# Kernel tuning notes

Measured on AMD Instinct MI355X. Metric: run time of the kernel, lower is better.

The kernel has to match this reference:

```python
import jax, jax.numpy as jnp
import numpy as np

E = 16        # num experts
D = 1024      # d_model
F = 512       # expert intermediate dim
B, S = 2, 2048


def setup_inputs() -> dict:
    key = jax.random.key(0)
    ks = jax.random.split(key, 8)
    sc = lambda fan_in: 1.0 / np.sqrt(fan_in)
    return {
        "x": jax.random.normal(ks[0], (B, S, D), dtype=jnp.float32),
        "router_w": jax.random.normal(ks[1], (E, D), dtype=jnp.float32) * sc(D),
        "gate_w": jax.random.normal(ks[2], (E, D, F), dtype=jnp.float32) * sc(D),
        "up_w": jax.random.normal(ks[3], (E, D, F), dtype=jnp.float32) * sc(D),
        "down_w": jax.random.normal(ks[4], (E, F, D), dtype=jnp.float32) * sc(F),
        "sg_w": jax.random.normal(ks[5], (D, F), dtype=jnp.float32) * sc(D),
        "su_w": jax.random.normal(ks[6], (D, F), dtype=jnp.float32) * sc(D),
        "sd_w": jax.random.normal(ks[7], (F, D), dtype=jnp.float32) * sc(F),
        "top_k": 8,
    }


def reference(x, router_w, gate_w, up_w, down_w, sg_w, su_w, sd_w, top_k):
    shape = x.shape
    xf = x.reshape(-1, shape[-1])                      # [T, D]
    # --- router: softmax then top-k, renormalize ---
    logits = xf.astype(jnp.float32) @ router_w.T       # [T, E]
    probs = jax.nn.softmax(logits, axis=-1)
    w, idx = jax.lax.top_k(probs, top_k)               # [T, k]
    w = w / jnp.sum(w, axis=-1, keepdims=True)
    # combine weight per (token, expert): sum over the k slots
    cw = jnp.sum(jax.nn.one_hot(idx, E, dtype=w.dtype) * w[..., None], axis=1)  # [T, E]
    # --- experts (dense batched SwiGLU, weighted combine) ---
    g = jnp.einsum("td,edf->etf", xf, gate_w)          # [E, T, F]
    u = jnp.einsum("td,edf->etf", xf, up_w)
    h = jax.nn.silu(g) * u
    out = jnp.einsum("etf,efd,te->td", h, down_w, cw)  # [T, D]
    # --- shared expert ---
    out = out + (jax.nn.silu(xf @ sg_w) * (xf @ su_w)) @ sd_w
    return out.reshape(shape)
```

## Files before the change

### kernel.cpp

```cpp
#include <hip/hip_runtime.h>
#include <hip/hip_bf16.h>

#define T_TOK 4096
#define DDIM  1024
#define FDIM  512
#define NEXP  16
#define NE17  17
#define MAXTILES 304

using bf16x8 = __attribute__((ext_vector_type(8))) __bf16;
using f32x4  = __attribute__((ext_vector_type(4))) float;

__device__ __forceinline__ void gload_lds16(const void* g, void* l) {
  __builtin_amdgcn_global_load_lds(
      (const __attribute__((address_space(1))) void*)g,
      (__attribute__((address_space(3))) void*)l, 16, 0, 0);
}

__device__ __forceinline__ bf16x8 frag_ld(const __hip_bfloat16* smem, int row, int chunk) {
  const char* p = (const char*)smem + row * 128 + ((chunk ^ (row & 7)) << 4);
  return *(const bf16x8*)p;
}

__global__ void convert_router(const float* __restrict__ x, const float* __restrict__ rw,
                               __hip_bfloat16* __restrict__ xb, float* __restrict__ cw) {
  const int t = blockIdx.x;
  const int lane = threadIdx.x;
  const float4* xrow = (const float4*)(x + (size_t)t * DDIM);
  float4 v[4];
#pragma unroll
  for (int c = 0; c < 4; c++) v[c] = xrow[lane + 64 * c];
  __hip_bfloat16* orow = xb + (size_t)t * DDIM;
#pragma unroll
  for (int c = 0; c < 4; c++) {
    __hip_bfloat16 h[4] = {__float2bfloat16(v[c].x), __float2bfloat16(v[c].y),
                           __float2bfloat16(v[c].z), __float2bfloat16(v[c].w)};
    *(uint2*)(orow + (lane + 64 * c) * 4) = *(const uint2*)h;
  }
  const float4* rw4 = (const float4*)rw;
  float myLg = 0.f;
#pragma unroll
  for (int e = 0; e < NEXP; e++) {
    float p = 0.f;
#pragma unroll
    for (int c = 0; c < 4; c++) {
      const float4 r = rw4[e * 256 + lane + 64 * c];
      p += v[c].x * r.x + v[c].y * r.y + v[c].z * r.z + v[c].w * r.w;
    }
#pragma unroll
    for (int off = 32; off > 0; off >>= 1) p += __shfl_xor(p, off);
    if (lane == e) myLg = p;
  }
  float m = myLg;
#pragma unroll
  for (int off = 8; off > 0; off >>= 1) m = fmaxf(m, __shfl_xor(m, off));
  const float pe = __expf(myLg - m);
  int rank = 0;
#pragma unroll
  for (int j = 0; j < NEXP; j++) {
    const float pj = __shfl(pe, j);
    rank += ((pj > pe) || (pj == pe && j < lane)) ? 1 : 0;
  }
  const bool sel = (lane < NEXP) && (rank < 8);
  float ss = sel ? pe : 0.f;
#pragma unroll
  for (int off = 8; off > 0; off >>= 1) ss += __shfl_xor(ss, off);
  if (lane < NEXP) cw[(size_t)t * NEXP + lane] = sel ? pe / ss : 0.f;
}

__global__ void moe_count(const float* __restrict__ cw, int* __restrict__ cnt) {
  const int e = blockIdx.x;
  const int lane = threadIdx.x;
  int c = 0;
  for (int t = lane; t < T_TOK; t += 64) c += (cw[(size_t)t * 16 + e] > 0.f) ? 1 : 0;
#pragma unroll
  for (int off = 32; off > 0; off >>= 1) c += __shfl_xor(c, off);
  if (lane == 0) cnt[e] = c;
}

__global__ void moe_scan(const int* __restrict__ cnt, int* __restrict__ padBase,
                         int* __restrict__ tileE, int* __restrict__ tileBase) {
  if (threadIdx.x != 0) return;
  int base = 0, tile = 0;
  for (int e = 0; e < 16; e++) {
    padBase[e] = base;
    const int nt = (cnt[e] + 127) >> 7;
    for (int i = 0; i < nt; i++) { tileE[tile] = e; tileBase[tile] = base + (i << 7); tile++; }
    base += nt << 7;
  }
  padBase[16] = base;
  for (int i = 0; i < 32; i++) { tileE[tile] = 16; tileBase[tile] = base + (i << 7); tile++; }
  for (; tile < MAXTILES; tile++) tileE[tile] = -1;
}

__global__ void moe_place(const float* __restrict__ cw, const int* __restrict__ cnt,
                          const int* __restrict__ padBase,
                          int* __restrict__ perm, float* __restrict__ rowW) {
  const int e = blockIdx.x;
  const int lane = threadIdx.x;
  const int base = padBase[e];
  if (e == 16) {
    for (int t = lane; t < T_TOK; t += 64) { perm[base + t] = t; rowW[base + t] = 1.0f; }
    return;
  }
  int running = 0;
  for (int t0 = 0; t0 < T_TOK; t0 += 64) {
    const int t = t0 + lane;
    const float w = cw[(size_t)t * 16 + e];
    const unsigned long long m = __ballot(w > 0.f);
    if (w > 0.f) {
      const int r = base + running + __popcll(m & ((1ull << lane) - 1ull));
      perm[r] = t; rowW[r] = w;
    }
    running += __popcll(m);
  }
  const int padded = ((cnt[e] + 127) >> 7) << 7;
  for (int i = running + lane; i < padded; i += 64) { perm[base + i] = -1; rowW[base + i] = 0.f; }
}

__global__ __launch_bounds__(256, 4) void transpose_convert2(
    const float* __restrict__ srcMainA, const float* __restrict__ srcSharedA,
    const float* __restrict__ srcMainB, const float* __restrict__ srcSharedB,
    __hip_bfloat16* __restrict__ dstA, __hip_bfloat16* __restrict__ dstB, int R, int C) {
  const int e = blockIdx.z;
  const float* srcA = (e < NEXP) ? srcMainA + (size_t)e * R * C : srcSharedA;
  const float* srcB = (e < NEXP) ? srcMainB + (size_t)e * R * C : srcSharedB;
  __hip_bfloat16* outA = dstA + (size_t)e * R * C;
  __hip_bfloat16* outB = dstB + (size_t)e * R * C;
  __shared__ float tA[64][65];
  __shared__ float tB[64][65];
  const int c0 = blockIdx.x * 64, r0 = blockIdx.y * 64;
  const int tx = threadIdx.x, ty = threadIdx.y;
#pragma unroll
  for (int i = 0; i < 64; i += 4) {
    tA[ty + i][tx] = srcA[(size_t)(r0 + ty + i) * C + c0 + tx];
    tB[ty + i][tx] = srcB[(size_t)(r0 + ty + i) * C + c0 + tx];
  }
  __syncthreads();
#pragma unroll
  for (int i = 0; i < 64; i += 4) {
    outA[(size_t)(c0 + ty + i) * R + r0 + tx] = __float2bfloat16(tA[tx][ty + i]);
    outB[(size_t)(c0 + ty + i) * R + r0 + tx] = __float2bfloat16(tB[tx][ty + i]);
  }
}

__global__ __launch_bounds__(256, 4) void transpose_convert(
    const float* __restrict__ srcMain, const float* __restrict__ srcShared,
    __hip_bfloat16* __restrict__ dst, int R, int C) {
  const int e = blockIdx.z;
  const float* src = (e < NEXP) ? srcMain + (size_t)e * R * C : srcShared;
  __hip_bfloat16* out = dst + (size_t)e * R * C;
  __shared__ float tile[64][65];
  const int c0 = blockIdx.x * 64, r0 = blockIdx.y * 64;
  const int tx = threadIdx.x, ty = threadIdx.y;
#pragma unroll
  for (int i = 0; i < 64; i += 4)
    tile[ty + i][tx] = src[(size_t)(r0 + ty + i) * C + c0 + tx];
  __syncthreads();
#pragma unroll
  for (int i = 0; i < 64; i += 4)
    out[(size_t)(c0 + ty + i) * R + r0 + tx] = __float2bfloat16(tile[tx][ty + i]);
}

__global__ __launch_bounds__(256, 3) void moe_stageA_grouped(
    const __hip_bfloat16* __restrict__ xb,
    const __hip_bfloat16* __restrict__ wg,
    const __hip_bfloat16* __restrict__ wu,
    const int* __restrict__ perm, const float* __restrict__ rowW,
    const int* __restrict__ tileE, const int* __restrict__ tileBase,
    __hip_bfloat16* __restrict__ H)
{
  __shared__ __hip_bfloat16 sA[128 * 64];
  __shared__ __hip_bfloat16 sG[64 * 64];
  __shared__ __hip_bfloat16 sU[64 * 64];
  __shared__ int   sTok[128];
  __shared__ float sW[128];

  const int tile = (blockIdx.x & 7) * (MAXTILES / 8) + (blockIdx.x >> 3);
  const int e = tileE[tile];
  if (e < 0) return;
  const int rbase = tileBase[tile];
  const int f0 = blockIdx.y * 64;
  const int tid = threadIdx.x;
  const int wid = tid >> 6, lane = tid & 63;
  const int wr = (wid >> 1) * 64, wc = (wid & 1) * 32;
  const int rl = lane >> 3, cl = lane & 7;

  if (tid < 128) { const int r = rbase + tid; sTok[tid] = perm[r]; sW[tid] = rowW[r]; }
  __syncthreads();

  const __hip_bfloat16* wgE = wg + (size_t)e * FDIM * DDIM;
  const __hip_bfloat16* wuE = wu + (size_t)e * FDIM * DDIM;

  const char* pA[4]; const char* pG[2]; const char* pU[2]; int ldsA[4], ldsB[2];
#pragma unroll
  for (int i = 0; i < 4; i++) {
    const int row = 32 * wid + 8 * i + rl;
    const int sw = (cl ^ (row & 7)) << 3;
    int tk = sTok[row]; if (tk < 0) tk = 0;
    pA[i] = (const char*)(xb + (size_t)tk * DDIM + sw);
    ldsA[i] = (32 * wid + 8 * i) * 64;
  }
#pragma unroll
  for (int i = 0; i < 2; i++) {
    const int row = 16 * wid + 8 * i + rl;
    const int sw = (cl ^ (row & 7)) << 3;
    pG[i] = (const char*)(wgE + (size_t)(f0 + row) * DDIM + sw);
    pU[i] = (const char*)(wuE + (size_t)(f0 + row) * DDIM + sw);
    ldsB[i] = (16 * wid + 8 * i) * 64;
  }

  const f32x4 vzero = {0.f, 0.f, 0.f, 0.f};
  f32x4 accG[4][2], accU[4][2];
#pragma unroll
  for (int m = 0; m < 4; m++)
#pragma unroll
    for (int n = 0; n < 2; n++) { accG[m][n] = vzero; accU[m][n] = vzero; }

  for (int k0 = 0; k0 < DDIM; k0 += 64) {
    __syncthreads();
#pragma unroll
    for (int i = 0; i < 4; i++) gload_lds16(pA[i] + (size_t)k0 * 2, &sA[ldsA[i]]);
#pragma unroll
    for (int i = 0; i < 2; i++) {
      gload_lds16(pG[i] + (size_t)k0 * 2, &sG[ldsB[i]]);
      gload_lds16(pU[i] + (size_t)k0 * 2, &sU[ldsB[i]]);
    }
    __syncthreads();
#pragma unroll
    for (int kk = 0; kk < 2; kk++) {
      const int kch = kk * 4 + (lane >> 4);
      bf16x8 af[4], bg[2], bu[2];
#pragma unroll
      for (int m = 0; m < 4; m++) af[m] = frag_ld(sA, wr + m * 16 + (lane & 15), kch);
#pragma unroll
      for (int n = 0; n < 2; n++) {
        bg[n] = frag_ld(sG, wc + n * 16 + (lane & 15), kch);
        bu[n] = frag_ld(sU, wc + n * 16 + (lane & 15), kch);
      }
#pragma unroll
      for (int m = 0; m < 4; m++)
#pragma unroll
        for (int n = 0; n < 2; n++) {
          accG[m][n] = __builtin_amdgcn_mfma_f32_16x16x32_bf16(af[m], bg[n], accG[m][n], 0, 0, 0);
          accU[m][n] = __builtin_amdgcn_mfma_f32_16x16x32_bf16(af[m], bu[n], accU[m][n], 0, 0, 0);
        }
    }
  }
  const int lr = (lane >> 4) * 4, lc = lane & 15;
#pragma unroll
  for (int m = 0; m < 4; m++)
#pragma unroll
    for (int n = 0; n < 2; n++)
#pragma unroll
      for (int j = 0; j < 4; j++) {
        const int r = wr + m * 16 + lr + j;
        const int c = wc + n * 16 + lc;
        const int tok = sTok[r];
        if (tok >= 0) {
          const float g = accG[m][n][j], u = accU[m][n][j];
          const float h = (g / (1.0f + __expf(-g))) * u * sW[r];
          H[((size_t)e * T_TOK + tok) * FDIM + f0 + c] = __float2bfloat16(h);
        }
      }
}

__global__ __launch_bounds__(256, 4) void moe_stageB_split(
    const __hip_bfloat16* __restrict__ H,
    const __hip_bfloat16* __restrict__ wd,
    float* __restrict__ out,
    float* __restrict__ p0, float* __restrict__ p1)
{
  __shared__ __hip_bfloat16 sA[128 * 64];
  __shared__ __hip_bfloat16 sB[128 * 64];

  const int id = blockIdx.x;
  const int xcd = id & 7, slot = id >> 3;
  const int t0 = (xcd * 4 + (slot & 3)) * 128;
  const int d0 = (slot >> 2) * 128;
  const int tid = threadIdx.x, wid = tid >> 6, lane = tid & 63;
  const int wr = (wid >> 1) * 64, wc = (wid & 1) * 64;
  const int rl = lane >> 3, cl = lane & 7;

  size_t offA[4], offB[4]; int ldsO[4];
#pragma unroll
  for (int i = 0; i < 4; i++) {
    const int row = 32 * wid + 8 * i + rl;
    const int sw = (cl ^ (row & 7)) << 3;
    offA[i] = (size_t)(t0 + row) * FDIM + sw;
    offB[i] = (size_t)(d0 + row) * FDIM + sw;
    ldsO[i] = (32 * wid + 8 * i) * 64;
  }

  const f32x4 vzero = {0.f, 0.f, 0.f, 0.f};
  f32x4 acc[4][4];
#pragma unroll
  for (int m = 0; m < 4; m++)
#pragma unroll
    for (int n = 0; n < 4; n++) acc[m][n] = vzero;

  const int NKS = NE17 * FDIM / 64;
  const int split = blockIdx.y;
  const int ks0 = (split * NKS) / 3, ks1 = ((split + 1) * NKS) / 3;

  for (int ks = ks0; ks < ks1; ks++) {
    const int k0 = ks * 64;
    const int ee = k0 >> 9, ff = k0 & 511;
    const size_t sOffA = (size_t)ee * T_TOK * FDIM + ff;
    const size_t sOffB = (size_t)ee * DDIM * FDIM + ff;
    __syncthreads();
#pragma unroll
    for (int i = 0; i < 4; i++) {
      gload_lds16(H  + sOffA + offA[i], &sA[ldsO[i]]);
      gload_lds16(wd + sOffB + offB[i], &sB[ldsO[i]]);
    }
    __syncthreads();
#pragma unroll
    for (int kk = 0; kk < 2; kk++) {
      const int kch = kk * 4 + (lane >> 4);
      bf16x8 af[4], bb[4];
#pragma unroll
      for (int m = 0; m < 4; m++) af[m] = frag_ld(sA, wr + m * 16 + (lane & 15), kch);
#pragma unroll
      for (int n = 0; n < 4; n++) bb[n] = frag_ld(sB, wc + n * 16 + (lane & 15), kch);
#pragma unroll
      for (int m = 0; m < 4; m++)
#pragma unroll
        for (int n = 0; n < 4; n++)
          acc[m][n] = __builtin_amdgcn_mfma_f32_16x16x32_bf16(af[m], bb[n], acc[m][n], 0, 0, 0);
    }
  }
  float* dst = (split == 0) ? p0 : (split == 1) ? p1 : out;
  const int lr = (lane >> 4) * 4, lc = lane & 15;
#pragma unroll
  for (int m = 0; m < 4; m++)
#pragma unroll
    for (int n = 0; n < 4; n++)
#pragma unroll
      for (int j = 0; j < 4; j++)
        dst[(size_t)(t0 + wr + m * 16 + lr + j) * DDIM + d0 + wc + n * 16 + lc] = acc[m][n][j];
}

__global__ void add_partial(float* __restrict__ out, const float* __restrict__ p0,
                            const float* __restrict__ p1, int n4) {
  int i = blockIdx.x * blockDim.x + threadIdx.x;
  if (i >= n4) return;
  float4 a = ((const float4*)out)[i];
  float4 b = ((const float4*)p0)[i];
  float4 c = ((const float4*)p1)[i];
  a.x += b.x + c.x; a.y += b.y + c.y; a.z += b.z + c.z; a.w += b.w + c.w;
  ((float4*)out)[i] = a;
}

extern "C" void kernel_launch(void* const* d_in, const int* in_sizes, int n_in,
                              void* d_out, int out_size, void* d_ws, size_t ws_size,
                              hipStream_t stream) {
  const float* x  = (const float*)d_in[0];
  const float* rw = (const float*)d_in[1];
  const float* gw = (const float*)d_in[2];
  const float* uw = (const float*)d_in[3];
  const float* dw = (const float*)d_in[4];
  const float* sg = (const float*)d_in[5];
  const float* su = (const float*)d_in[6];
  const float* sd = (const float*)d_in[7];
  float* out = (float*)d_out;

  char* ws = (char*)d_ws;
  size_t off = 0;
  __hip_bfloat16* xb = (__hip_bfloat16*)(ws + off); off += (size_t)T_TOK * DDIM * 2;
  __hip_bfloat16* wg = (__hip_bfloat16*)(ws + off); off += (size_t)NE17 * FDIM * DDIM * 2;
  __hip_bfloat16* wu = (__hip_bfloat16*)(ws + off);
  const size_t wu_off = off;                         off += (size_t)NE17 * FDIM * DDIM * 2;
  __hip_bfloat16* wd = (__hip_bfloat16*)(ws + off);  off += (size_t)NE17 * DDIM * FDIM * 2;
  __hip_bfloat16* H  = (__hip_bfloat16*)(ws + off);
  const size_t H_bytes = (size_t)NE17 * T_TOK * FDIM * 2; off += H_bytes;
  float* cw      = (float*)(ws + off); off += (size_t)T_TOK * 16 * 4;
  int*   cnt     = (int*)(ws + off);   off += 32 * 4;
  int*   padBase = (int*)(ws + off);   off += 32 * 4;
  int*   tileE   = (int*)(ws + off);   off += MAXTILES * 4;
  int*   tileBase= (int*)(ws + off);   off += MAXTILES * 4;
  int*   perm    = (int*)(ws + off);   off += 40960 * 4;
  float* rowW    = (float*)(ws + off); off += 40960 * 4;
  float* p0 = (float*)ws;
  float* p1 = (float*)(ws + wu_off);
  (void)ws_size; (void)in_sizes; (void)n_in; (void)out_size;

  hipMemsetAsync(H, 0, H_bytes, stream);

  convert_router<<<T_TOK, 64, 0, stream>>>(x, rw, xb, cw);
  dim3 tb(64, 4);
  transpose_convert2<<<dim3(FDIM / 64, DDIM / 64, NE17), tb, 0, stream>>>(
      gw, sg, uw, su, wg, wu, DDIM, FDIM);
  transpose_convert<<<dim3(DDIM / 64, FDIM / 64, NE17), tb, 0, stream>>>(dw, sd, wd, FDIM, DDIM);

  moe_count<<<NEXP, 64, 0, stream>>>(cw, cnt);
  moe_scan<<<1, 64, 0, stream>>>(cnt, padBase, tileE, tileBase);
  moe_place<<<NE17, 64, 0, stream>>>(cw, cnt, padBase, perm, rowW);

  moe_stageA_grouped<<<dim3(MAXTILES, FDIM / 64), 256, 0, stream>>>(
      xb, wg, wu, perm, rowW, tileE, tileBase, H);
  moe_stageB_split<<<dim3(256, 3), 256, 0, stream>>>(H, wd, out, p0, p1);
  add_partial<<<(T_TOK * DDIM / 4 + 255) / 256, 256, 0, stream>>>(out, p0, p1, T_TOK * DDIM / 4);
}
```

Baseline: 264.4 us.

## Make down-projection grouped over routed rows and combine via token-to-row map

Stage A now writes H in compact padded per-expert row order instead of a dense [E,T,F] buffer, so the large memset of H is no longer needed. A new grouped stage B runs the down projection only on the routed tiles and writes per-row fp32 partials. A combine kernel then gathers the 8 expert rows plus the shared row for each token using a tok2row map built from a router selection mask. This drops the dense 17-expert K reduction and the split-K partial adds, at the cost of a large fp32 partial buffer (40960x1024) and an extra gather pass. The new path runs only when the workspace is big enough; otherwise the old path is used.

Measured after the change: 282.4 us. 6.8% more time.

```diff
diff --git a/kernel.cpp b/kernel.cpp
--- a/kernel.cpp
+++ b/kernel.cpp
@@ -7,6 +7,7 @@
 #define NEXP  16
 #define NE17  17
 #define MAXTILES 304
+#define MAXROWS  40960
 
 using bf16x8 = __attribute__((ext_vector_type(8))) __bf16;
 using f32x4  = __attribute__((ext_vector_type(4))) float;
@@ -23,7 +24,8 @@
 }
 
 __global__ void convert_router(const float* __restrict__ x, const float* __restrict__ rw,
-                               __hip_bfloat16* __restrict__ xb, float* __restrict__ cw) {
+                               __hip_bfloat16* __restrict__ xb, float* __restrict__ cw,
+                               unsigned* __restrict__ selMask) {
   const int t = blockIdx.x;
   const int lane = threadIdx.x;
   const float4* xrow = (const float4*)(x + (size_t)t * DDIM);
@@ -62,10 +64,12 @@
     rank += ((pj > pe) || (pj == pe && j < lane)) ? 1 : 0;
   }
   const bool sel = (lane < NEXP) && (rank < 8);
+  const unsigned mask = (unsigned)(__ballot(sel) & 0xFFFFull);
   float ss = sel ? pe : 0.f;
 #pragma unroll
   for (int off = 8; off > 0; off >>= 1) ss += __shfl_xor(ss, off);
   if (lane < NEXP) cw[(size_t)t * NEXP + lane] = sel ? pe / ss : 0.f;
+  if (lane == 0) selMask[t] = mask;
 }
 
 __global__ void moe_count(const float* __restrict__ cw, int* __restrict__ cnt) {
@@ -94,8 +98,9 @@
 }
 
 __global__ void moe_place(const float* __restrict__ cw, const int* __restrict__ cnt,
-                          const int* __restrict__ padBase,
-                          int* __restrict__ perm, float* __restrict__ rowW) {
+                          const int* __restrict__ padBase, const unsigned* __restrict__ selMask,
+                          int* __restrict__ perm, float* __restrict__ rowW,
+                          int* __restrict__ tok2row) {
   const int e = blockIdx.x;
   const int lane = threadIdx.x;
   const int base = padBase[e];
@@ -111,6 +116,8 @@
     if (w > 0.f) {
       const int r = base + running + __popcll(m & ((1ull << lane) - 1ull));
       perm[r] = t; rowW[r] = w;
+      const int slot = __popc(selMask[t] & ((1u << e) - 1u));
+      tok2row[t * 8 + slot] = r;
     }
     running += __popcll(m);
   }
@@ -168,7 +175,7 @@
     const __hip_bfloat16* __restrict__ wu,
     const int* __restrict__ perm, const float* __restrict__ rowW,
     const int* __restrict__ tileE, const int* __restrict__ tileBase,
-    __hip_bfloat16* __restrict__ H)
+    __hip_bfloat16* __restrict__ H, int groupedStore)
 {
   __shared__ __hip_bfloat16 sA[128 * 64];
   __shared__ __hip_bfloat16 sG[64 * 64];
@@ -260,20 +267,108 @@
         if (tok >= 0) {
           const float g = accG[m][n][j], u = accU[m][n][j];
           const float h = (g / (1.0f + __expf(-g))) * u * sW[r];
-          H[((size_t)e * T_TOK + tok) * FDIM + f0 + c] = __float2bfloat16(h);
+          const size_t idx = groupedStore
+              ? ((size_t)(rbase + r) * FDIM + f0 + c)
+              : (((size_t)e * T_TOK + tok) * FDIM + f0 + c);
+          H[idx] = __float2bfloat16(h);
         }
       }
+}
+
+__global__ __launch_bounds__(256, 4) void moe_stageB_grouped(
+    const __hip_bfloat16* __restrict__ Hp,
+    const __hip_bfloat16* __restrict__ wd,
+    const int* __restrict__ tileE, const int* __restrict__ tileBase,
+    float* __restrict__ outp)
+{
+  __shared__ __hip_bfloat16 sA[128 * 64];
+  __shared__ __hip_bfloat16 sB[128 * 64];
+
+  const int tile = (blockIdx.x & 7) * (MAXTILES / 8) + (blockIdx.x >> 3);
+  const int e = tileE[tile];
+  if (e < 0) return;
+  const int rbase = tileBase[tile];
+  const int d0 = blockIdx.y * 128;
+  const int tid = threadIdx.x, wid = tid >> 6, lane = tid & 63;
+  const int wr = (wid >> 1) * 64, wc = (wid & 1) * 64;
+  const int rl = lane >> 3, cl = lane & 7;
+
+  const __hip_bfloat16* wdE = wd + (size_t)e * DDIM * FDIM;
+
+  size_t offA[4], offB[4]; int ldsO[4];
+#pragma unroll
+  for (int i = 0; i < 4; i++) {
+    const int row = 32 * wid + 8 * i + rl;
+    const int sw = (cl ^ (row & 7)) << 3;
+    offA[i] = (size_t)(rbase + row) * FDIM + sw;
+    offB[i] = (size_t)(d0 + row) * FDIM + sw;
+    ldsO[i] = (32 * wid + 8 * i) * 64;
+  }
+
+  const f32x4 vzero = {0.f, 0.f, 0.f, 0.f};
+  f32x4 acc[4][4];
+#pragma unroll
+  for (int m = 0; m < 4; m++)
+#pragma unroll
+    for (int n = 0; n < 4; n++) acc[m][n] = vzero;
+
+  for (int k0 = 0; k0 < FDIM; k0 += 64) {
+    __syncthreads();
+#pragma unroll
+    for (int i = 0; i < 4; i++) {
+      gload_lds16(Hp  + offA[i] + k0, &sA[ldsO[i]]);
+      gload_lds16(wdE + offB[i] + k0, &sB[ldsO[i]]);
+    }
+    __syncthreads();
+#pragma unroll
+    for (int kk = 0; kk < 2; kk++) {
+      const int kch = kk * 4 + (lane >> 4);
+      bf16x8 af[4], bb[4];
+#pragma unroll
+      for (int m = 0; m < 4; m++) af[m] = frag_ld(sA, wr + m * 16 + (lane & 15), kch);
+#pragma unroll
+      for (int n = 0; n < 4; n++) bb[n] = frag_ld(sB, wc + n * 16 + (lane & 15), kch);
+#pragma unroll
+      for (int m = 0; m < 4; m++)
+#pragma unroll
+        for (int n = 0; n < 4; n++)
+          acc[m][n] = __builtin_amdgcn_mfma_f32_16x16x32_bf16(af[m], bb[n], acc[m][n], 0, 0, 0);
+    }
+  }
+  const int lr = (lane >> 4) * 4, lc = lane & 15;
+#pragma unroll
+  for (int m = 0; m < 4; m++)
+#pragma unroll
+    for (int n = 0; n < 4; n++)
+#pragma unroll
+      for (int j = 0; j < 4; j++)
+        outp[(size_t)(rbase + wr + m * 16 + lr + j) * DDIM + d0 + wc + n * 16 + lc]
+            = acc[m][n][j];
+}
+
+__global__ void moe_combine(const float* __restrict__ outp, const int* __restrict__ tok2row,
+                            const int* __restrict__ padBase, float* __restrict__ out) {
+  const int t = blockIdx.x;
+  const int tid = threadIdx.x;
+  const float4* o4 = (const float4*)outp;
+  const int sharedRow = padBase[16] + t;
+  float4 a = o4[(size_t)sharedRow * (DDIM / 4) + tid];
+#pragma unroll
+  for (int s = 0; s < 8; s++) {
+    const int r = tok2row[t * 8 + s];
+    const float4 b = o4[(size_t)r * (DDIM / 4) + tid];
+    a.x += b.x; a.y += b.y; a.z += b.z; a.w += b.w;
+  }
+  ((float4*)out)[(size_t)t * (DDIM / 4) + tid] = a;
 }
 
 __global__ __launch_bounds__(256, 4) void moe_stageB_split(
     const __hip_bfloat16* __restrict__ H,
     const __hip_bfloat16* __restrict__ wd,
-    float* __restrict__ out,
-    float* __restrict__ p0, float* __restrict__ p1)
+    float* __restrict__ out, float* __restrict__ p0, float* __restrict__ p1)
 {
   __shared__ __hip_bfloat16 sA[128 * 64];
   __shared__ __hip_bfloat16 sB[128 * 64];
-
   const int id = blockIdx.x;
   const int xcd = id & 7, slot = id >> 3;
   const int t0 = (xcd * 4 + (slot & 3)) * 128;
@@ -281,7 +376,6 @@
   const int tid = threadIdx.x, wid = tid >> 6, lane = tid & 63;
   const int wr = (wid >> 1) * 64, wc = (wid & 1) * 64;
   const int rl = lane >> 3, cl = lane & 7;
-
   size_t offA[4], offB[4]; int ldsO[4];
 #pragma unroll
   for (int i = 0; i < 4; i++) {
@@ -291,18 +385,15 @@
     offB[i] = (size_t)(d0 + row) * FDIM + sw;
     ldsO[i] = (32 * wid + 8 * i) * 64;
   }
-
   const f32x4 vzero = {0.f, 0.f, 0.f, 0.f};
   f32x4 acc[4][4];
 #pragma unroll
   for (int m = 0; m < 4; m++)
 #pragma unroll
     for (int n = 0; n < 4; n++) acc[m][n] = vzero;
-
   const int NKS = NE17 * FDIM / 64;
   const int split = blockIdx.y;
   const int ks0 = (split * NKS) / 3, ks1 = ((split + 1) * NKS) / 3;
-
   for (int ks = ks0; ks < ks1; ks++) {
     const int k0 = ks * 64;
     const int ee = k0 >> 9, ff = k0 & 511;
@@ -379,15 +470,20 @@
   int*   padBase = (int*)(ws + off);   off += 32 * 4;
   int*   tileE   = (int*)(ws + off);   off += MAXTILES * 4;
   int*   tileBase= (int*)(ws + off);   off += MAXTILES * 4;
-  int*   perm    = (int*)(ws + off);   off += 40960 * 4;
-  float* rowW    = (float*)(ws + off); off += 40960 * 4;
+  int*   perm    = (int*)(ws + off);   off += MAXROWS * 4;
+  float* rowW    = (float*)(ws + off); off += MAXROWS * 4;
+  unsigned* selMask = (unsigned*)(ws + off); off += (size_t)T_TOK * 4;
+  int*   tok2row = (int*)(ws + off);   off += (size_t)T_TOK * 8 * 4;
+  const size_t outp_bytes = (size_t)MAXROWS * DDIM * 4;
+  float* outp = (float*)(ws + off);
+  const bool grouped = (ws_size >= off + outp_bytes);
   float* p0 = (float*)ws;
   float* p1 = (float*)(ws + wu_off);
-  (void)ws_size; (void)in_sizes; (void)n_in; (void)out_size;
-
-  hipMemsetAsync(H, 0, H_bytes, stream);
-
-  convert_router<<<T_TOK, 64, 0, stream>>>(x, rw, xb, cw);
+  (void)in_sizes; (void)n_in; (void)out_size;
+
+  if (!grouped) hipMemsetAsync(H, 0, H_bytes, stream);
+
+  convert_router<<<T_TOK, 64, 0, stream>>>(x, rw, xb, cw, selMask);
   dim3 tb(64, 4);
   transpose_convert2<<<dim3(FDIM / 64, DDIM / 64, NE17), tb, 0, stream>>>(
       gw, sg, uw, su, wg, wu, DDIM, FDIM);
@@ -395,10 +491,17 @@
 
   moe_count<<<NEXP, 64, 0, stream>>>(cw, cnt);
   moe_scan<<<1, 64, 0, stream>>>(cnt, padBase, tileE, tileBase);
-  moe_place<<<NE17, 64, 0, stream>>>(cw, cnt, padBase, perm, rowW);
+  moe_place<<<NE17, 64, 0, stream>>>(cw, cnt, padBase, selMask, perm, rowW, tok2row);
 
   moe_stageA_grouped<<<dim3(MAXTILES, FDIM / 64), 256, 0, stream>>>(
-      xb, wg, wu, perm, rowW, tileE, tileBase, H);
-  moe_stageB_split<<<dim3(256, 3), 256, 0, stream>>>(H, wd, out, p0, p1);
-  add_partial<<<(T_TOK * DDIM / 4 + 255) / 256, 256, 0, stream>>>(out, p0, p1, T_TOK * DDIM / 4);
-}
+      xb, wg, wu, perm, rowW, tileE, tileBase, H, grouped ? 1 : 0);
+
+  if (grouped) {
+    moe_stageB_grouped<<<dim3(MAXTILES, DDIM / 128), 256, 0, stream>>>(
+        H, wd, tileE, tileBase, outp);
+    moe_combine<<<T_TOK, 256, 0, stream>>>(outp, tok2row, padBase, out);
+  } else {
+    moe_stageB_split<<<dim3(256, 3), 256, 0, stream>>>(H, wd, out, p0, p1);
+    add_partial<<<(T_TOK * DDIM / 4 + 255) / 256, 256, 0, stream>>>(out, p0, p1, T_TOK * DDIM / 4);
+  }
+}
```
